# Performance work log

Hardware: AMD Instinct MI355X
Metric: run time of the kernel (lower is better)

## Reference

```python
import jax, jax.numpy as jnp
import numpy as np

KERNEL_NUM = 21
SIGMA = 0.1
EXACT_SIGMA = 0.001
VOCAB, EMB_DIM = 50000, 128
B, LQ, LD = 1024, 64, 256
EPS = 1e-12  # torch F.normalize eps


def _kernel_params():
    # mus: midpoints of linspace(-1,1,21) via convolve with [0.5,0.5], trimmed -> 20 values
    mus = np.convolve(np.linspace(-1.0, 1.0, KERNEL_NUM), np.array([0.5, 0.5]))[1:-1]
    mus = np.concatenate([mus, np.array([1.0])])            # + exact-match kernel
    sigmas = np.concatenate([np.full(KERNEL_NUM - 1, SIGMA), np.array([EXACT_SIGMA])])
    return jnp.asarray(mus, jnp.float32), jnp.asarray(sigmas, jnp.float32)


def setup_inputs() -> dict:
    key = jax.random.key(0)
    ks = jax.random.split(key, 9)
    emb = jax.random.normal(ks[0], (VOCAB, EMB_DIM), jnp.float32)
    emb = emb.at[0].set(0.0)  # padding_idx=0 row is zero
    return {
        "query": jax.random.randint(ks[1], (B, LQ), 0, VOCAB),
        "document": jax.random.randint(ks[2], (B, LD), 0, VOCAB),
        "emb": emb,
        "W1": jax.random.normal(ks[3], (10, 21), jnp.float32) * 0.2,
        "b1": jax.random.normal(ks[4], (10,), jnp.float32) * 0.1,
        "W2": jax.random.normal(ks[5], (5, 10), jnp.float32) * 0.2,
        "b2": jax.random.normal(ks[6], (5,), jnp.float32) * 0.1,
        "W3": jax.random.normal(ks[7], (1, 5), jnp.float32) * 0.2,
        "b3": jax.random.normal(ks[8], (1,), jnp.float32) * 0.1,
    }


def _l2norm(x):
    n = jnp.linalg.norm(x, axis=-1, keepdims=True)
    return x / jnp.maximum(n, EPS)


def reference(query, document, emb, W1, b1, W2, b2, W3, b3):
    mus, sigmas = _kernel_params()
    q = _l2norm(emb[query])                       # [B, Lq, E]
    d = _l2norm(emb[document])                    # [B, Ld, E]
    mm = jnp.einsum("bqe,bde->bqd", q, d)         # cosine matching matrix [B, Lq, Ld]
    # all 21 Gaussian kernels in one pass: [B, Lq, Ld, K]
    diff = mm[..., None] - mus
    kvals = jnp.exp(-(diff * diff) / (2.0 * sigmas * sigmas))
    km = jnp.log1p(kvals.sum(axis=2)).sum(axis=1)  # sum over doc, log1p, sum over query -> [B, K]
    x = jax.nn.relu(km)
    x = jax.nn.relu(x @ W1.T + b1)
    x = x @ W2.T + b2
    return x @ W3.T + b3                           # [B, 1]
```

## Files before the change

kernel.cpp:

```cpp
#include <hip/hip_runtime.h>
#include <hip/hip_bf16.h>

#define L2E 1.4426950408889634f
#define LN2 0.6931471805599453f

#if defined(__has_builtin)
#if __has_builtin(__builtin_amdgcn_exp2f)
#define EXP2(x) __builtin_amdgcn_exp2f(x)
#else
#define EXP2(x) exp2f(x)
#endif
#if __has_builtin(__builtin_amdgcn_logf)
#define LOG2(x) __builtin_amdgcn_logf(x)
#else
#define LOG2(x) __log2f(x)
#endif
#else
#define EXP2(x) exp2f(x)
#define LOG2(x) __log2f(x)
#endif

typedef __attribute__((ext_vector_type(8))) short bf16x8;
typedef __attribute__((ext_vector_type(4))) float f32x4;
typedef __attribute__((ext_vector_type(2))) float f32x2;

__device__ __forceinline__ void gld_lds16(const void* g, void* l) {
  __builtin_amdgcn_global_load_lds(
      (const __attribute__((address_space(1))) void*)g,
      (__attribute__((address_space(3))) void*)l, 16, 0, 0);
}

__device__ __forceinline__ unsigned bf16rne(float f) {
  unsigned u = __float_as_uint(f);
  return (u + 0x7fffu + ((u >> 16) & 1u)) >> 16;
}

__global__ __launch_bounds__(256) void knrm_norm(const float* __restrict__ emb,
                                                 unsigned* __restrict__ embN) {
  const int t = threadIdx.x;
  const int l = t & 31;
  const int sub = (t >> 5) & 1;
  int wv = blockIdx.x * 4 + (t >> 6);
  const int nW = gridDim.x * 4;
  for (int rp = wv; rp < 25000; rp += nW) {
    int r = rp * 2 + sub;
    float4 v = *(const float4*)(emb + (size_t)r * 128 + l * 4);
    float ss = v.x * v.x + v.y * v.y + v.z * v.z + v.w * v.w;
#pragma unroll
    for (int m = 1; m < 32; m <<= 1) ss += __shfl_xor(ss, m, 64);
    float sc = 1.0f / fmaxf(sqrtf(ss), 1e-12f);
    uint2 o;
    o.x = bf16rne(v.x * sc) | (bf16rne(v.y * sc) << 16);
    o.y = bf16rne(v.z * sc) | (bf16rne(v.w * sc) << 16);
    *(uint2*)(embN + (size_t)r * 64 + l * 2) = o;
  }
}

__global__ __launch_bounds__(256, 4) void knrm_main(
    const int* __restrict__ query, const int* __restrict__ doc,
    const unsigned* __restrict__ embN,
    const float* __restrict__ W1, const float* __restrict__ b1,
    const float* __restrict__ W2, const float* __restrict__ b2,
    const float* __restrict__ W3, const float* __restrict__ b3,
    float* __restrict__ out) {
  __shared__ __align__(16) char dbuf[2][64 * 256];
  __shared__ float kmbuf[64 * 21];
  __shared__ int dtok[256];
  __shared__ float km2[4][21];
  __shared__ float kmv[21];
  __shared__ float x1[10];
  __shared__ float x2[5];

  const int b = blockIdx.x;
  const int tid = threadIdx.x;
  const int w = tid >> 6;
  const int lane = tid & 63;
  const int lo = lane & 15, hi = lane >> 4;
  const char* embB = (const char*)embN;

  dtok[tid] = doc[b * 256 + tid];

  const int myq = query[b * 64 + w * 16 + lo];
  bf16x8 bq[4];
#pragma unroll
  for (int kk = 0; kk < 4; ++kk)
    bq[kk] = *(const bf16x8*)(embB + (size_t)myq * 256 + kk * 64 + hi * 16);

#pragma unroll
  for (int it = 0; it < 4; ++it) {
    int rl = w * 16 + it * 4 + hi;
    int tok = doc[b * 256 + rl];
    int slot = lo ^ (rl & 7);
    gld_lds16(embB + (size_t)tok * 256 + slot * 16, dbuf[0] + (w * 16 + it * 4) * 256);
  }
  asm volatile("s_waitcnt vmcnt(0)" ::: "memory");
  __syncthreads();

  f32x2 acc20[20];
#pragma unroll
  for (int j = 0; j < 20; ++j) acc20[j] = (f32x2){0.0f, 0.0f};

#pragma unroll 1
  for (int qtr = 0; qtr < 4; ++qtr) {
    const int cur = qtr & 1;
    if (qtr < 3) {
#pragma unroll
      for (int it = 0; it < 4; ++it) {
        int rl = w * 16 + it * 4 + hi;
        int tok = doc[b * 256 + (qtr + 1) * 64 + rl];
        int slot = lo ^ (rl & 7);
        gld_lds16(embB + (size_t)tok * 256 + slot * 16,
                  dbuf[cur ^ 1] + (w * 16 + it * 4) * 256);
      }
    }
#pragma unroll
    for (int dr = 0; dr < 4; ++dr) {
      f32x4 mm = {0.0f, 0.0f, 0.0f, 0.0f};
#pragma unroll
      for (int kk = 0; kk < 4; ++kk) {
        int row = dr * 16 + lo;
        int slot = (kk * 4 + hi) ^ (lo & 7);
        bf16x8 a = *(const bf16x8*)(dbuf[cur] + row * 256 + slot * 16);
        mm = __builtin_amdgcn_mfma_f32_16x16x32_bf16(a, bq[kk], mm, 0, 0, 0);
      }
#pragma unroll
      for (int p = 0; p < 2; ++p) {
        f32x2 v = {mm[p], mm[p + 2]};
        f32x2 m = v * L2E;
        f32x2 a10 = m * 10.0f;
        f32x2 G, Gi, t9;
        G.x = EXP2(a10.x);
        G.y = EXP2(a10.y);
        Gi.x = EXP2(-a10.x);
        Gi.y = EXP2(-a10.y);
        f32x2 e9 = m * (v * -50.0f - 5.0f);
        t9.x = EXP2(e9.x);
        t9.y = EXP2(e9.y);
        f32x2 tu = t9, td = t9;
        acc20[9] += t9;
#pragma unroll
        for (int j = 10; j < 20; ++j) { tu *= G; acc20[j] += tu; }
#pragma unroll
        for (int j = 8; j >= 0; --j) { td *= Gi; acc20[j] += td; }
      }
    }
    asm volatile("s_waitcnt vmcnt(0)" ::: "memory");
    __syncthreads();
  }

  int cnt = 0;
#pragma unroll 16
  for (int i = 0; i < 64; ++i) cnt += (dtok[hi * 64 + i] == myq) ? 1 : 0;
  cnt = (myq == 0) ? 0 : cnt;

  float sa[20];
#pragma unroll
  for (int j = 0; j < 20; ++j) {
    float s = acc20[j].x + acc20[j].y;
    s += __shfl_xor(s, 16, 64);
    s += __shfl_xor(s, 32, 64);
    sa[j] = s;
  }
  cnt += __shfl_xor(cnt, 16, 64);
  cnt += __shfl_xor(cnt, 32, 64);

  if (hi == 0) {
    int q = w * 16 + lo;
#pragma unroll
    for (int j = 0; j < 20; ++j) kmbuf[q * 21 + j] = sa[j];
    kmbuf[q * 21 + 20] = (float)cnt;
  }
  __syncthreads();

  const float cA = -50.0f * L2E;
  if (tid < 84) {
    int j = tid % 21, c = tid / 21;
    float Cj = 1.0f;
    if (j < 20) {
      float mu = -0.95f + 0.1f * (float)j;
      Cj = EXP2(cA * mu * mu);
    }
    float s = 0.0f;
    for (int q = 0; q < 16; ++q)
      s += LOG2(fmaf(Cj, kmbuf[(c * 16 + q) * 21 + j], 1.0f));
    km2[c][j] = s * LN2;
  }
  __syncthreads();
  if (tid < 21)
    kmv[tid] = fmaxf(km2[0][tid] + km2[1][tid] + km2[2][tid] + km2[3][tid], 0.0f);
  __syncthreads();
  if (tid < 10) {
    float s = b1[tid];
    for (int j = 0; j < 21; ++j) s = fmaf(W1[tid * 21 + j], kmv[j], s);
    x1[tid] = fmaxf(s, 0.0f);
  }
  __syncthreads();
  if (tid < 5) {
    float s = b2[tid];
    for (int i = 0; i < 10; ++i) s = fmaf(W2[tid * 10 + i], x1[i], s);
    x2[tid] = s;
  }
  __syncthreads();
  if (tid == 0) {
    float s = b3[0];
    for (int i = 0; i < 5; ++i) s = fmaf(W3[i], x2[i], s);
    out[b] = s;
  }
}

extern "C" void kernel_launch(void* const* d_in, const int* in_sizes, int n_in,
                              void* d_out, int out_size, void* d_ws, size_t ws_size,
                              hipStream_t stream) {
  const int* query = (const int*)d_in[0];
  const int* doc = (const int*)d_in[1];
  const float* emb = (const float*)d_in[2];
  const float* W1 = (const float*)d_in[3];
  const float* b1 = (const float*)d_in[4];
  const float* W2 = (const float*)d_in[5];
  const float* b2 = (const float*)d_in[6];
  const float* W3 = (const float*)d_in[7];
  const float* b3 = (const float*)d_in[8];
  float* out = (float*)d_out;
  unsigned* embN = (unsigned*)d_ws;

  hipLaunchKernelGGL(knrm_norm, dim3(1024), dim3(256), 0, stream, emb, embN);
  hipLaunchKernelGGL(knrm_main, dim3(1024), dim3(256), 0, stream, query, doc, embN,
                     W1, b1, W2, b2, W3, b3, out);
}
```

Baseline: 40.23 us.

## Split each block's document rows across two wave groups with 512 threads

The main kernel now launches 512 threads per block. Two groups of four waves each take a different 16-row half of a 32-row document chunk, and the block steps through eight smaller double-buffered chunks instead of four. Per-group kernel sums go to separate shared buffers and are added before the log step. This doubles the waves available to hide latency and halves the LDS staging buffer, at the cost of twice as many block barriers and more per-wave query-fragment loads.

```diff
diff --git a/kernel.cpp b/kernel.cpp
--- a/kernel.cpp
+++ b/kernel.cpp
@@ -56,15 +56,15 @@
   }
 }
 
-__global__ __launch_bounds__(256, 4) void knrm_main(
+__global__ __launch_bounds__(512, 8) void knrm_main(
     const int* __restrict__ query, const int* __restrict__ doc,
     const unsigned* __restrict__ embN,
     const float* __restrict__ W1, const float* __restrict__ b1,
     const float* __restrict__ W2, const float* __restrict__ b2,
     const float* __restrict__ W3, const float* __restrict__ b3,
     float* __restrict__ out) {
-  __shared__ __align__(16) char dbuf[2][64 * 256];
-  __shared__ float kmbuf[64 * 21];
+  __shared__ __align__(16) char dbuf[2][32 * 256];
+  __shared__ float kmbuf[2][64][21];
   __shared__ int dtok[256];
   __shared__ float km2[4][21];
   __shared__ float kmv[21];
@@ -76,22 +76,23 @@
   const int w = tid >> 6;
   const int lane = tid & 63;
   const int lo = lane & 15, hi = lane >> 4;
+  const int qs = w & 3;
+  const int g = w >> 2;
   const char* embB = (const char*)embN;
 
-  dtok[tid] = doc[b * 256 + tid];
-
-  const int myq = query[b * 64 + w * 16 + lo];
+  if (tid < 256) dtok[tid] = doc[b * 256 + tid];
+
+  const int myq = query[b * 64 + qs * 16 + lo];
   bf16x8 bq[4];
 #pragma unroll
   for (int kk = 0; kk < 4; ++kk)
     bq[kk] = *(const bf16x8*)(embB + (size_t)myq * 256 + kk * 64 + hi * 16);
 
-#pragma unroll
-  for (int it = 0; it < 4; ++it) {
-    int rl = w * 16 + it * 4 + hi;
-    int tok = doc[b * 256 + rl];
-    int slot = lo ^ (rl & 7);
-    gld_lds16(embB + (size_t)tok * 256 + slot * 16, dbuf[0] + (w * 16 + it * 4) * 256);
+  const int srow = w * 4 + (lane >> 4);
+  const int sslot = (lane & 15) ^ (srow & 7);
+  {
+    int tok = doc[b * 256 + srow];
+    gld_lds16(embB + (size_t)tok * 256 + sslot * 16, dbuf[0] + w * 1024);
   }
   asm volatile("s_waitcnt vmcnt(0)" ::: "memory");
   __syncthreads();
@@ -101,74 +102,67 @@
   for (int j = 0; j < 20; ++j) acc20[j] = (f32x2){0.0f, 0.0f};
 
 #pragma unroll 1
-  for (int qtr = 0; qtr < 4; ++qtr) {
-    const int cur = qtr & 1;
-    if (qtr < 3) {
-#pragma unroll
-      for (int it = 0; it < 4; ++it) {
-        int rl = w * 16 + it * 4 + hi;
-        int tok = doc[b * 256 + (qtr + 1) * 64 + rl];
-        int slot = lo ^ (rl & 7);
-        gld_lds16(embB + (size_t)tok * 256 + slot * 16,
-                  dbuf[cur ^ 1] + (w * 16 + it * 4) * 256);
-      }
-    }
-#pragma unroll
-    for (int dr = 0; dr < 4; ++dr) {
-      f32x4 mm = {0.0f, 0.0f, 0.0f, 0.0f};
-#pragma unroll
-      for (int kk = 0; kk < 4; ++kk) {
-        int row = dr * 16 + lo;
-        int slot = (kk * 4 + hi) ^ (lo & 7);
-        bf16x8 a = *(const bf16x8*)(dbuf[cur] + row * 256 + slot * 16);
-        mm = __builtin_amdgcn_mfma_f32_16x16x32_bf16(a, bq[kk], mm, 0, 0, 0);
-      }
-#pragma unroll
-      for (int p = 0; p < 2; ++p) {
-        f32x2 v = {mm[p], mm[p + 2]};
-        f32x2 m = v * L2E;
-        f32x2 a10 = m * 10.0f;
-        f32x2 G, Gi, t9;
-        G.x = EXP2(a10.x);
-        G.y = EXP2(a10.y);
-        Gi.x = EXP2(-a10.x);
-        Gi.y = EXP2(-a10.y);
-        f32x2 e9 = m * (v * -50.0f - 5.0f);
-        t9.x = EXP2(e9.x);
-        t9.y = EXP2(e9.y);
-        f32x2 tu = t9, td = t9;
-        acc20[9] += t9;
-#pragma unroll
-        for (int j = 10; j < 20; ++j) { tu *= G; acc20[j] += tu; }
-#pragma unroll
-        for (int j = 8; j >= 0; --j) { td *= Gi; acc20[j] += td; }
-      }
+  for (int s = 0; s < 8; ++s) {
+    const int cur = s & 1;
+    if (s < 7) {
+      int tok = doc[b * 256 + (s + 1) * 32 + srow];
+      gld_lds16(embB + (size_t)tok * 256 + sslot * 16, dbuf[cur ^ 1] + w * 1024);
+    }
+    f32x4 mm = {0.0f, 0.0f, 0.0f, 0.0f};
+#pragma unroll
+    for (int kk = 0; kk < 4; ++kk) {
+      int row = g * 16 + lo;
+      int slot = (kk * 4 + hi) ^ (lo & 7);
+      bf16x8 a = *(const bf16x8*)(dbuf[cur] + row * 256 + slot * 16);
+      mm = __builtin_amdgcn_mfma_f32_16x16x32_bf16(a, bq[kk], mm, 0, 0, 0);
+    }
+#pragma unroll
+    for (int p = 0; p < 2; ++p) {
+      f32x2 v = {mm[p], mm[p + 2]};
+      f32x2 m = v * L2E;
+      f32x2 a10 = m * 10.0f;
+      f32x2 G, Gi, t9;
+      G.x = EXP2(a10.x);
+      G.y = EXP2(a10.y);
+      Gi.x = EXP2(-a10.x);
+      Gi.y = EXP2(-a10.y);
+      f32x2 e9 = m * (v * -50.0f - 5.0f);
+      t9.x = EXP2(e9.x);
+      t9.y = EXP2(e9.y);
+      f32x2 tu = t9, td = t9;
+      acc20[9] += t9;
+#pragma unroll
+      for (int j = 10; j < 20; ++j) { tu *= G; acc20[j] += tu; }
+#pragma unroll
+      for (int j = 8; j >= 0; --j) { td *= Gi; acc20[j] += td; }
     }
     asm volatile("s_waitcnt vmcnt(0)" ::: "memory");
     __syncthreads();
   }
 
   int cnt = 0;
+  if (g == 0) {
 #pragma unroll 16
-  for (int i = 0; i < 64; ++i) cnt += (dtok[hi * 64 + i] == myq) ? 1 : 0;
-  cnt = (myq == 0) ? 0 : cnt;
+    for (int i = 0; i < 64; ++i) cnt += (dtok[hi * 64 + i] == myq) ? 1 : 0;
+    cnt = (myq == 0) ? 0 : cnt;
+    cnt += __shfl_xor(cnt, 16, 64);
+    cnt += __shfl_xor(cnt, 32, 64);
+  }
 
   float sa[20];
 #pragma unroll
   for (int j = 0; j < 20; ++j) {
-    float s = acc20[j].x + acc20[j].y;
-    s += __shfl_xor(s, 16, 64);
-    s += __shfl_xor(s, 32, 64);
-    sa[j] = s;
-  }
-  cnt += __shfl_xor(cnt, 16, 64);
-  cnt += __shfl_xor(cnt, 32, 64);
+    float s2 = acc20[j].x + acc20[j].y;
+    s2 += __shfl_xor(s2, 16, 64);
+    s2 += __shfl_xor(s2, 32, 64);
+    sa[j] = s2;
+  }
 
   if (hi == 0) {
-    int q = w * 16 + lo;
-#pragma unroll
-    for (int j = 0; j < 20; ++j) kmbuf[q * 21 + j] = sa[j];
-    kmbuf[q * 21 + 20] = (float)cnt;
+    int q = qs * 16 + lo;
+#pragma unroll
+    for (int j = 0; j < 20; ++j) kmbuf[g][q][j] = sa[j];
+    kmbuf[g][q][20] = (g == 0) ? (float)cnt : 0.0f;
   }
   __syncthreads();
 
@@ -181,8 +175,10 @@
       Cj = EXP2(cA * mu * mu);
     }
     float s = 0.0f;
-    for (int q = 0; q < 16; ++q)
-      s += LOG2(fmaf(Cj, kmbuf[(c * 16 + q) * 21 + j], 1.0f));
+    for (int q = 0; q < 16; ++q) {
+      float raw = kmbuf[0][c * 16 + q][j] + kmbuf[1][c * 16 + q][j];
+      s += LOG2(fmaf(Cj, raw, 1.0f));
+    }
     km2[c][j] = s * LN2;
   }
   __syncthreads();
@@ -224,6 +220,6 @@
   unsigned* embN = (unsigned*)d_ws;
 
   hipLaunchKernelGGL(knrm_norm, dim3(1024), dim3(256), 0, stream, emb, embN);
-  hipLaunchKernelGGL(knrm_main, dim3(1024), dim3(256), 0, stream, query, doc, embN,
+  hipLaunchKernelGGL(knrm_main, dim3(1024), dim3(512), 0, stream, query, doc, embN,
                      W1, b1, W2, b2, W3, b3, out);
 }
```

Result: slower. 75.17 us (+86.9%).
